# Kernel optimization log

Hardware: AMD Instinct MI355X
Metric: run time of the kernel (lower is better)

The kernel has to match this reference:

```python
import jax, jax.numpy as jnp
import numpy as np

GROUP = 64      # SVDQuant hard-coded group size
QMAX = 7.0      # symmetric int4: values in [-8, 7], scale = max|x| / 7
EPS = 1e-8


def setup_inputs() -> dict:
    key = jax.random.key(0)
    k0, k1, k2, k3, k4 = jax.random.split(key, 5)
    T, K, N, R = 4096, 4096, 4096, 32  # tokens, in_features, out_features, rank

    x = jax.random.normal(k0, (T, K), jnp.float32)

    # Full-precision weight, decomposed offline into low-rank + int4 residual
    w = jax.random.normal(k1, (N, K), jnp.float32) * 0.02
    proj_down = jax.random.normal(k2, (K, R), jnp.float32) * 0.02  # x @ proj_down -> [T, R]
    proj_up = jax.random.normal(k3, (R, N), jnp.float32) * 0.02    # [T, R] @ proj_up -> [T, N]
    residual = w - (proj_down @ proj_up).T  # [N, K]

    # Symmetric per-group int4 quantization of the residual weight
    rg = residual.reshape(N, K // GROUP, GROUP)
    wscales = jnp.maximum(jnp.max(jnp.abs(rg), axis=-1) / QMAX, EPS)  # [N, K/G]
    q_w = jnp.clip(jnp.round(rg / wscales[..., None]), -8, 7).astype(jnp.int8).reshape(N, K)

    smooth = jnp.ones((K,), jnp.float32)  # load_from_replicated sets smooth to ones
    bias = jax.random.normal(k4, (N,), jnp.float32) * 0.02
    return {
        "x": x,
        "q_w": q_w,
        "wscales": wscales,
        "proj_down": proj_down,
        "proj_up": proj_up,
        "smooth": smooth,
        "bias": bias,
    }


def reference(x, q_w, wscales, proj_down, proj_up, smooth, bias):
    T, K = x.shape
    N = q_w.shape[0]

    # smoothing (identity here, per load_from_replicated)
    xs = x * smooth

    # low-rank SVD correction branch (full precision)
    lr = (xs @ proj_down) @ proj_up  # [T, N]

    # W4A4 branch: symmetric per-token per-group int4 activation quantization
    xg = xs.reshape(T, K // GROUP, GROUP)
    ascales = jnp.maximum(jnp.max(jnp.abs(xg), axis=-1) / QMAX, EPS)  # [T, K/G]
    q_x = jnp.clip(jnp.round(xg / ascales[..., None]), -8.0, 7.0)
    x_dq = (q_x * ascales[..., None]).reshape(T, K)  # dequantized activations

    # dequantize int4 weights with per-(out_channel, group) scales
    w_dq = (q_w.astype(jnp.float32).reshape(N, K // GROUP, GROUP)
            * wscales[..., None]).reshape(N, K)

    # fused dequant-matmul + low-rank add + bias
    return lr + x_dq @ w_dq.T + bias
```

## Files before the change

kernel.cpp:

```cpp
#include <hip/hip_runtime.h>
#include <hip/hip_bf16.h>
#include <stdint.h>

#define Tdim 4096
#define Ndim 4096
#define Kdim 4096
#define K2   4160

using f32x4  = __attribute__((ext_vector_type(4))) float;
using bf16x8 = __attribute__((ext_vector_type(8))) short;

__device__ inline ushort f2bf(float f) {
  union { float f; unsigned u; } v; v.f = f;
  unsigned lsb = (v.u >> 16) & 1u;
  v.u += 0x7fffu + lsb;
  return (ushort)(v.u >> 16);
}

__device__ inline unsigned pack2(float a, float b) {
  return (unsigned)f2bf(a) | ((unsigned)f2bf(b) << 16);
}

__device__ inline float qd(float v, float s) {
  return fminf(fmaxf(rintf(v / s), -8.f), 7.f) * s;
}

__device__ inline void async16(const void* g, void* l) {
  __builtin_amdgcn_global_load_lds(
      (const __attribute__((address_space(1))) unsigned int*)g,
      (__attribute__((address_space(3))) unsigned int*)l, 16, 0, 0);
}

__global__ __launch_bounds__(256) void prep_a_kernel(
    const float* __restrict__ x, const float* __restrict__ smooth,
    const float* __restrict__ pd, ushort* __restrict__ A,
    float* __restrict__ partials) {
  __shared__ __attribute__((aligned(16))) ushort sXS[128 * 136];
  __shared__ __attribute__((aligned(16))) ushort sQ[128 * 136];
  const int tid  = threadIdx.x;
  const int lane = tid & 63;
  const int wave = tid >> 6;
  const int fr  = lane & 15;
  const int fkq = lane >> 4;
  const int fk  = fkq * 8;
  const int tok0 = blockIdx.x * 128;
  const int kc0  = blockIdx.y * 512;
  const int r = tid >> 1;
  const int g = tid & 1;
  const int srow2 = tid >> 2;
  const int scol2 = (tid & 3) * 8;

  f32x4 acc[2][2] = {};

  for (int c = 0; c < 4; ++c) {
    const int kbase = kc0 + c * 128;
    const int kcol  = g * 64;
    const float4* xp = (const float4*)&x[(size_t)(tok0 + r) * Kdim + kbase + kcol];
    const float4* sp = (const float4*)&smooth[kbase + kcol];
    float4 v[16];
#pragma unroll
    for (int q = 0; q < 16; ++q) {
      float4 xv = xp[q], sm = sp[q];
      v[q].x = xv.x * sm.x; v[q].y = xv.y * sm.y;
      v[q].z = xv.z * sm.z; v[q].w = xv.w * sm.w;
    }
    float a = 0.f;
#pragma unroll
    for (int q = 0; q < 16; ++q)
      a = fmaxf(a, fmaxf(fmaxf(fabsf(v[q].x), fabsf(v[q].y)),
                         fmaxf(fabsf(v[q].z), fabsf(v[q].w))));
    const float s = fmaxf(a / 7.0f, 1e-8f);
#pragma unroll
    for (int q2 = 0; q2 < 8; ++q2) {
      const float4 v0 = v[2 * q2], v1 = v[2 * q2 + 1];
      uint4 wx, wq;
      wx.x = pack2(v0.x, v0.y);           wx.y = pack2(v0.z, v0.w);
      wx.z = pack2(v1.x, v1.y);           wx.w = pack2(v1.z, v1.w);
      wq.x = pack2(qd(v0.x, s), qd(v0.y, s)); wq.y = pack2(qd(v0.z, s), qd(v0.w, s));
      wq.z = pack2(qd(v1.x, s), qd(v1.y, s)); wq.w = pack2(qd(v1.z, s), qd(v1.w, s));
      *(uint4*)&sXS[r * 136 + kcol + q2 * 8] = wx;
      *(uint4*)&sQ [r * 136 + kcol + q2 * 8] = wq;
    }
    __syncthreads();

#pragma unroll
    for (int kk = 0; kk < 4; ++kk) {
      bf16x8 af0 = *(const bf16x8*)&sXS[(wave * 32 + fr) * 136 + kk * 32 + fk];
      bf16x8 af1 = *(const bf16x8*)&sXS[(wave * 32 + 16 + fr) * 136 + kk * 32 + fk];
      bf16x8 b0, b1;
#pragma unroll
      for (int e = 0; e < 8; ++e) {
        const size_t kr = (size_t)(kbase + kk * 32 + fk + e) * 32;
        b0[e] = (short)f2bf(pd[kr + fr]);
        b1[e] = (short)f2bf(pd[kr + 16 + fr]);
      }
      acc[0][0] = __builtin_amdgcn_mfma_f32_16x16x32_bf16(af0, b0, acc[0][0], 0, 0, 0);
      acc[0][1] = __builtin_amdgcn_mfma_f32_16x16x32_bf16(af0, b1, acc[0][1], 0, 0, 0);
      acc[1][0] = __builtin_amdgcn_mfma_f32_16x16x32_bf16(af1, b0, acc[1][0], 0, 0, 0);
      acc[1][1] = __builtin_amdgcn_mfma_f32_16x16x32_bf16(af1, b1, acc[1][1], 0, 0, 0);
    }

#pragma unroll
    for (int h = 0; h < 2; ++h) {
      const int rr = srow2 + h * 64;
#pragma unroll
      for (int u = 0; u < 4; ++u)
        *(uint4*)&A[(size_t)(tok0 + rr) * K2 + kbase + scol2 + u * 32] =
            *(const uint4*)&sQ[rr * 136 + scol2 + u * 32];
    }
    __syncthreads();
  }

  float* P = partials + (size_t)blockIdx.y * Tdim * 32;
#pragma unroll
  for (int i = 0; i < 2; ++i) {
    const int row0 = tok0 + wave * 32 + i * 16 + fkq * 4;
#pragma unroll
    for (int j = 0; j < 2; ++j) {
      const int col = j * 16 + fr;
#pragma unroll
      for (int rr = 0; rr < 4; ++rr)
        P[(size_t)(row0 + rr) * 32 + col] = acc[i][j][rr];
    }
  }
}

__global__ __launch_bounds__(256) void wprep_kernel(
    const int* __restrict__ qw, const float* __restrict__ wsc,
    const float* __restrict__ partials, const float* __restrict__ pu,
    ushort* __restrict__ A, ushort* __restrict__ B) {
  const int bid = blockIdx.x;
  if (bid < 8192) {
    const size_t idx = ((size_t)bid * 256 + threadIdx.x) * 8;
    const int n = (int)(idx >> 12);
    const int k = (int)(idx & 4095);
    const float s = wsc[n * 64 + (k >> 6)];
    const int4 q0 = *(const int4*)(qw + idx);
    const int4 q1 = *(const int4*)(qw + idx + 4);
    uint4 o;
    o.x = pack2((float)q0.x * s, (float)q0.y * s);
    o.y = pack2((float)q0.z * s, (float)q0.w * s);
    o.z = pack2((float)q1.x * s, (float)q1.y * s);
    o.w = pack2((float)q1.z * s, (float)q1.w * s);
    *(uint4*)(B + (size_t)n * K2 + k) = o;
  } else if (bid < 8192 + 1024) {
    const int idx = (bid - 8192) * 256 + threadIdx.x;
    const int token = idx >> 6, c = idx & 63;
    ushort v = 0;
    if (c < 32) {
      float s = 0.f;
#pragma unroll
      for (int p = 0; p < 8; ++p)
        s += partials[(size_t)p * Tdim * 32 + (size_t)token * 32 + c];
      v = f2bf(s);
    }
    A[(size_t)token * K2 + Kdim + c] = v;
  } else {
    const int idx = (bid - 9216) * 256 + threadIdx.x;
    const int n = idx >> 6, c = idx & 63;
    ushort v = 0;
    if (c < 32) v = f2bf(pu[(size_t)c * Ndim + n]);
    B[(size_t)n * K2 + Kdim + c] = v;
  }
}

__global__ __launch_bounds__(256) void gemm_kernel(
    const ushort* __restrict__ A, const ushort* __restrict__ B,
    const float* __restrict__ bias, float* __restrict__ C) {
  __shared__ __attribute__((aligned(16))) ushort sA[2 * 128 * 32];
  __shared__ __attribute__((aligned(16))) ushort sB[2 * 128 * 32];
  const int tid  = threadIdx.x;
  const int lane = tid & 63;
  const int wave = tid >> 6;
  const int wr = (wave >> 1) * 64;
  const int wc = (wave & 1) * 64;
  const int fr = lane & 15;
  const size_t arow0 = (size_t)blockIdx.x * 128;
  const size_t brow0 = (size_t)blockIdx.y * 128;
  const int srow = tid >> 2;
  const int cs   = tid & 3;
  const int skc  = (cs ^ ((srow >> 1) & 3)) * 8;
  const int fchunk = (((lane >> 4) ^ ((fr >> 1) & 3))) * 8;

  const ushort* gA = A + (arow0 + srow) * K2 + skc;
  const ushort* gB = B + (brow0 + srow) * K2 + skc;

  f32x4 acc[4][4] = {};

  for (int k0 = 0; k0 < K2; k0 += 64) {
#pragma unroll
    for (int p = 0; p < 2; ++p) {
      async16(gA + p * 32,                   &sA[p * 4096 + tid * 8]);
      async16(gA + p * 32 + (size_t)64 * K2, &sA[p * 4096 + (tid + 256) * 8]);
      async16(gB + p * 32,                   &sB[p * 4096 + tid * 8]);
      async16(gB + p * 32 + (size_t)64 * K2, &sB[p * 4096 + (tid + 256) * 8]);
    }
    gA += 64; gB += 64;
    __syncthreads();

#pragma unroll
    for (int kk = 0; kk < 2; ++kk) {
      bf16x8 af[4], bfr[4];
#pragma unroll
      for (int i = 0; i < 4; ++i)
        af[i] = *(const bf16x8*)&sA[kk * 4096 + (wr + i * 16 + fr) * 32 + fchunk];
#pragma unroll
      for (int j = 0; j < 4; ++j)
        bfr[j] = *(const bf16x8*)&sB[kk * 4096 + (wc + j * 16 + fr) * 32 + fchunk];
#pragma unroll
      for (int i = 0; i < 4; ++i)
#pragma unroll
        for (int j = 0; j < 4; ++j)
          acc[i][j] = __builtin_amdgcn_mfma_f32_16x16x32_bf16(af[i], bfr[j], acc[i][j], 0, 0, 0);
    }
    __syncthreads();
  }

  const int rq = (lane >> 4) * 4;
#pragma unroll
  for (int j = 0; j < 4; ++j) {
    const size_t col = brow0 + wc + j * 16 + fr;
    const float bv = bias[col];
#pragma unroll
    for (int i = 0; i < 4; ++i) {
      const size_t row = arow0 + wr + i * 16 + rq;
#pragma unroll
      for (int r = 0; r < 4; ++r)
        C[(row + r) * Ndim + col] = acc[i][j][r] + bv;
    }
  }
}

extern "C" void kernel_launch(void* const* d_in, const int* in_sizes, int n_in,
                              void* d_out, int out_size, void* d_ws, size_t ws_size,
                              hipStream_t stream) {
  const float* x      = (const float*)d_in[0];
  const int*   qw     = (const int*)d_in[1];
  const float* wsc    = (const float*)d_in[2];
  const float* pd     = (const float*)d_in[3];
  const float* pu     = (const float*)d_in[4];
  const float* smooth = (const float*)d_in[5];
  const float* bias   = (const float*)d_in[6];
  float* out = (float*)d_out;

  const size_t abytes = (size_t)Tdim * K2 * 2;
  ushort* A    = (ushort*)d_ws;
  ushort* B    = (ushort*)((char*)d_ws + abytes);
  float*  part = (float*)((char*)d_ws + 2 * abytes);

  hipLaunchKernelGGL(prep_a_kernel, dim3(32, 8),  dim3(256), 0, stream, x, smooth, pd, A, part);
  hipLaunchKernelGGL(wprep_kernel,  dim3(10240),  dim3(256), 0, stream, qw, wsc, part, pu, A, B);
  hipLaunchKernelGGL(gemm_kernel,   dim3(32, 32), dim3(256), 0, stream, A, B, bias, out);
}
```

Baseline: 371.1 us.

## Pre-transpose proj_down to bf16, double K-split in prep, swizzle GEMM tile order

Adds a small kernel that converts proj_down to a transposed bf16 layout, so the prep kernel loads MFMA B fragments as contiguous 16-byte vectors. Before, it did strided scalar fp32 loads and per-element bf16 conversion. The prep kernel's K-split grows from 8 to 16 chunks to raise parallelism, which doubles the partial-sum reduction work. The GEMM remaps block indices into 8x8 supertiles to improve L2 reuse of A and B. Costs are one extra launch and more partial-sum traffic.

```diff
diff --git a/kernel.cpp b/kernel.cpp
--- a/kernel.cpp
+++ b/kernel.cpp
@@ -6,6 +6,7 @@
 #define Ndim 4096
 #define Kdim 4096
 #define K2   4160
+#define NSPLIT 16
 
 using f32x4  = __attribute__((ext_vector_type(4))) float;
 using bf16x8 = __attribute__((ext_vector_type(8))) short;
@@ -31,9 +32,17 @@
       (__attribute__((address_space(3))) unsigned int*)l, 16, 0, 0);
 }
 
+__global__ __launch_bounds__(256) void prep_pdT_kernel(
+    const float* __restrict__ pd, ushort* __restrict__ pdT) {
+  const int idx = blockIdx.x * 256 + threadIdx.x;
+  const int n = idx >> 12;
+  const int k = idx & 4095;
+  pdT[(size_t)n * Kdim + k] = f2bf(pd[(size_t)k * 32 + n]);
+}
+
 __global__ __launch_bounds__(256) void prep_a_kernel(
     const float* __restrict__ x, const float* __restrict__ smooth,
-    const float* __restrict__ pd, ushort* __restrict__ A,
+    const ushort* __restrict__ pdT, ushort* __restrict__ A,
     float* __restrict__ partials) {
   __shared__ __attribute__((aligned(16))) ushort sXS[128 * 136];
   __shared__ __attribute__((aligned(16))) ushort sQ[128 * 136];
@@ -44,7 +53,7 @@
   const int fkq = lane >> 4;
   const int fk  = fkq * 8;
   const int tok0 = blockIdx.x * 128;
-  const int kc0  = blockIdx.y * 512;
+  const int kc0  = blockIdx.y * 256;
   const int r = tid >> 1;
   const int g = tid & 1;
   const int srow2 = tid >> 2;
@@ -52,7 +61,7 @@
 
   f32x4 acc[2][2] = {};
 
-  for (int c = 0; c < 4; ++c) {
+  for (int c = 0; c < 2; ++c) {
     const int kbase = kc0 + c * 128;
     const int kcol  = g * 64;
     const float4* xp = (const float4*)&x[(size_t)(tok0 + r) * Kdim + kbase + kcol];
@@ -85,15 +94,11 @@
 
 #pragma unroll
     for (int kk = 0; kk < 4; ++kk) {
+      const int kglob = kbase + kk * 32 + fk;
       bf16x8 af0 = *(const bf16x8*)&sXS[(wave * 32 + fr) * 136 + kk * 32 + fk];
       bf16x8 af1 = *(const bf16x8*)&sXS[(wave * 32 + 16 + fr) * 136 + kk * 32 + fk];
-      bf16x8 b0, b1;
-#pragma unroll
-      for (int e = 0; e < 8; ++e) {
-        const size_t kr = (size_t)(kbase + kk * 32 + fk + e) * 32;
-        b0[e] = (short)f2bf(pd[kr + fr]);
-        b1[e] = (short)f2bf(pd[kr + 16 + fr]);
-      }
+      bf16x8 b0 = *(const bf16x8*)&pdT[(size_t)fr * Kdim + kglob];
+      bf16x8 b1 = *(const bf16x8*)&pdT[(size_t)(16 + fr) * Kdim + kglob];
       acc[0][0] = __builtin_amdgcn_mfma_f32_16x16x32_bf16(af0, b0, acc[0][0], 0, 0, 0);
       acc[0][1] = __builtin_amdgcn_mfma_f32_16x16x32_bf16(af0, b1, acc[0][1], 0, 0, 0);
       acc[1][0] = __builtin_amdgcn_mfma_f32_16x16x32_bf16(af1, b0, acc[1][0], 0, 0, 0);
@@ -150,7 +155,7 @@
     if (c < 32) {
       float s = 0.f;
 #pragma unroll
-      for (int p = 0; p < 8; ++p)
+      for (int p = 0; p < NSPLIT; ++p)
         s += partials[(size_t)p * Tdim * 32 + (size_t)token * 32 + c];
       v = f2bf(s);
     }
@@ -175,8 +180,15 @@
   const int wr = (wave >> 1) * 64;
   const int wc = (wave & 1) * 64;
   const int fr = lane & 15;
-  const size_t arow0 = (size_t)blockIdx.x * 128;
-  const size_t brow0 = (size_t)blockIdx.y * 128;
+
+  const int bid    = blockIdx.y * 32 + blockIdx.x;
+  const int super  = bid >> 6;
+  const int within = bid & 63;
+  const int brow   = (super >> 2) * 8 + (within >> 3);
+  const int bcol   = (super & 3) * 8 + (within & 7);
+  const size_t arow0 = (size_t)brow * 128;
+  const size_t brow0 = (size_t)bcol * 128;
+
   const int srow = tid >> 2;
   const int cs   = tid & 3;
   const int skc  = (cs ^ ((srow >> 1) & 3)) * 8;
@@ -246,9 +258,11 @@
   const size_t abytes = (size_t)Tdim * K2 * 2;
   ushort* A    = (ushort*)d_ws;
   ushort* B    = (ushort*)((char*)d_ws + abytes);
-  float*  part = (float*)((char*)d_ws + 2 * abytes);
-
-  hipLaunchKernelGGL(prep_a_kernel, dim3(32, 8),  dim3(256), 0, stream, x, smooth, pd, A, part);
-  hipLaunchKernelGGL(wprep_kernel,  dim3(10240),  dim3(256), 0, stream, qw, wsc, part, pu, A, B);
-  hipLaunchKernelGGL(gemm_kernel,   dim3(32, 32), dim3(256), 0, stream, A, B, bias, out);
-}
+  ushort* pdT  = (ushort*)((char*)d_ws + 2 * abytes);
+  float*  part = (float*)((char*)d_ws + 2 * abytes + 262144);
+
+  hipLaunchKernelGGL(prep_pdT_kernel, dim3(512),    dim3(256), 0, stream, pd, pdT);
+  hipLaunchKernelGGL(prep_a_kernel,   dim3(32, NSPLIT), dim3(256), 0, stream, x, smooth, pdT, A, part);
+  hipLaunchKernelGGL(wprep_kernel,    dim3(10240),  dim3(256), 0, stream, qw, wsc, part, pu, A, B);
+  hipLaunchKernelGGL(gemm_kernel,     dim3(32, 32), dim3(256), 0, stream, A, B, bias, out);
+}
```

New measurement: 357.8 us. 1.04x faster.
